# Performance work log

Hardware: AMD Instinct MI355X
Metric: run time of the kernel (lower is better)

## Reference

```python
import jax, jax.numpy as jnp
import numpy as np

B, M, D = 16384, 9, 512
DELTA = 0.5


def setup_inputs() -> dict:
    key = jax.random.key(0)
    k0, k1, k2, k3, k4 = jax.random.split(key, 5)
    s = 1.0 / np.sqrt(D).astype(np.float32)
    return {
        "x": jax.random.normal(k0, (B, M, D), jnp.float32),
        "Wi": jax.random.normal(k1, (M, D, D), jnp.float32) * s,
        "bi": jax.random.normal(k2, (M, D), jnp.float32) * s,
        "We": jax.random.normal(k3, (M, D, D), jnp.float32) * s,
        "be": jax.random.normal(k4, (M, D), jnp.float32) * s,
    }


def reference(x, Wi, bi, We, be):
    # ---- IntraRM: per-branch Linear+Sigmoid, L1-norm gating ----
    # batched per-branch GEMM: [B,M,D] x [M,D,D] -> [B,M,D]
    f = jax.nn.sigmoid(jnp.einsum('bmd,mde->bme', x, Wi) + bi)
    alphas = jnp.sum(jnp.abs(f), axis=-1)          # [B, M]  (L1 norm)
    feats = alphas[:, :, None] * x                  # [B, M, D]
    # ---- InterRM: per-branch Linear+ReLU, cdist affinity, tanh-masked matmul ----
    g = jax.nn.relu(jnp.einsum('bmd,mde->bme', feats, We) + be)  # [B, M, D]
    sq = jnp.sum(g * g, axis=-1)                    # [B, M]
    d2 = sq[:, :, None] + sq[:, None, :] - 2.0 * jnp.einsum('bmd,bnd->bmn', g, g)
    d2 = jnp.maximum(d2, 0.0)
    # safe sqrt (torch.cdist, p=2); diagonal d2==0 handled without NaN grads
    dist = jnp.where(d2 > 0, jnp.sqrt(jnp.where(d2 > 0, d2, 1.0)), 0.0)
    mask = 1.0 - jnp.eye(M, dtype=g.dtype)          # zero self-affinity
    affin = jnp.tanh(dist) * mask                   # [B, M, M]
    g_hat = jnp.einsum('bmn,bnd->bmd', affin, g)    # aggregate across branches
    out = DELTA * g + (1.0 - DELTA) * g_hat
    return out, alphas
```

## Files before the change

kernel.cpp:

```cpp
#include <hip/hip_runtime.h>
#include <hip/hip_bf16.h>
#include <hip/hip_fp16.h>

#define BATCH 16384
#define NM 9
#define ND 512
#define BM 64
#define NKT 16
#define NTHREADS 512
#define WMAT ((size_t)ND * ND)

typedef __bf16 bf16x8 __attribute__((ext_vector_type(8)));
typedef float  f32x4  __attribute__((ext_vector_type(4)));

__global__ __launch_bounds__(256)
void prep_weights(const float* __restrict__ Wi, const float* __restrict__ We,
                  __hip_bfloat16* __restrict__ WiT, __hip_bfloat16* __restrict__ WeT) {
  const int z  = blockIdx.y;
  const int kt = blockIdx.x;
  const float* src;
  __hip_bfloat16* dst;
  if (z < NM) { src = Wi + (size_t)z * WMAT;        dst = WiT + (size_t)z * WMAT; }
  else        { src = We + (size_t)(z - NM) * WMAT; dst = WeT + (size_t)(z - NM) * WMAT; }
  const int wave = threadIdx.x >> 6;
  const int lane = threadIdx.x & 63;
  const int k0   = kt * 32 + (lane >> 4) * 8;
  #pragma unroll
  for (int g = wave; g < 32; g += 4) {
    const int col = g * 16 + (lane & 15);
    bf16x8 v;
    #pragma unroll
    for (int j = 0; j < 8; ++j)
      v[j] = (__bf16)src[(size_t)(k0 + j) * ND + col];
    *(bf16x8*)(dst + (size_t)(kt * 32 + g) * 512 + lane * 8) = v;
  }
}

__global__ __launch_bounds__(NTHREADS, 4)
void gemm_kernel(const float* __restrict__ x,
                 const __hip_bfloat16* __restrict__ WiT,
                 const __hip_bfloat16* __restrict__ WeT,
                 const float* __restrict__ bi,
                 const float* __restrict__ be,
                 float* __restrict__ out) {
  __shared__ union {
    __hip_bfloat16 xs[BM][ND + 8];
    __half         gs[BM][ND + 8];
  } sh;
  __shared__ float alphaW[8][BM];
  __shared__ float alphaV[BM];

  const int tid  = threadIdx.x;
  const int wave = tid >> 6;
  const int lane = tid & 63;
  const int l15  = lane & 15;
  const int l4   = lane >> 4;

  const int bid = blockIdx.x;
  const int q   = bid >> 3;
  const int m   = q >> 5;
  const int bx  = (bid & 7) + ((q & 31) << 3);
  const int b0  = bx * BM;
  const int wn0 = wave * 64;

  float* alpha_out = out + (size_t)BATCH * NM * ND;

  const __hip_bfloat16* bpi = WiT + (size_t)m * WMAT + (size_t)wave * 4 * 512 + lane * 8;
  const __hip_bfloat16* bpe = WeT + (size_t)m * WMAT + (size_t)wave * 4 * 512 + lane * 8;

  bf16x8 breg[3][4];
  bf16x8 afr[2][4];

  #pragma unroll
  for (int d = 0; d < 3; ++d)
    #pragma unroll
    for (int nt = 0; nt < 4; ++nt)
      breg[d][nt] = *(const bf16x8*)(bpi + (size_t)d * 16384 + nt * 512);

  #pragma unroll
  for (int it = 0; it < (BM * ND / 4) / NTHREADS; ++it) {
    int idx = it * NTHREADS + tid;
    int r   = idx >> 7;
    int c4  = (idx & 127) * 4;
    float4 v = *(const float4*)(x + (size_t)(b0 + r) * (NM * ND) + m * ND + c4);
    union { ushort4 u; __hip_bfloat16 h[4]; } p;
    p.h[0] = __float2bfloat16(v.x);
    p.h[1] = __float2bfloat16(v.y);
    p.h[2] = __float2bfloat16(v.z);
    p.h[3] = __float2bfloat16(v.w);
    *(ushort4*)&sh.xs[r][c4] = p.u;
  }
  __syncthreads();

  f32x4 acc[4][4];
  #pragma unroll
  for (int a = 0; a < 4; ++a)
    #pragma unroll
    for (int c = 0; c < 4; ++c) acc[a][c] = (f32x4){0.f, 0.f, 0.f, 0.f};

  #pragma unroll
  for (int mt = 0; mt < 4; ++mt)
    afr[0][mt] = *(const bf16x8*)&sh.xs[mt * 16 + l15][l4 * 8];

  #pragma unroll
  for (int kt = 0; kt < NKT; ++kt) {
    if (kt + 1 < NKT) {
      const int kb = (kt + 1) * 32 + l4 * 8;
      #pragma unroll
      for (int mt = 0; mt < 4; ++mt)
        afr[(kt + 1) & 1][mt] = *(const bf16x8*)&sh.xs[mt * 16 + l15][kb];
    }
    #pragma unroll
    for (int mt = 0; mt < 4; ++mt)
      #pragma unroll
      for (int nt = 0; nt < 4; ++nt)
        acc[mt][nt] = __builtin_amdgcn_mfma_f32_16x16x32_bf16(afr[kt & 1][mt], breg[kt % 3][nt], acc[mt][nt], 0, 0, 0);
    if (kt + 3 < NKT) {
      const size_t off = (size_t)(kt + 3) * 16384;
      #pragma unroll
      for (int nt = 0; nt < 4; ++nt)
        breg[kt % 3][nt] = *(const bf16x8*)(bpi + off + nt * 512);
    }
  }

  #pragma unroll
  for (int d = 0; d < 3; ++d)
    #pragma unroll
    for (int nt = 0; nt < 4; ++nt)
      breg[d][nt] = *(const bf16x8*)(bpe + (size_t)d * 16384 + nt * 512);

  {
    float biv[4];
    #pragma unroll
    for (int nt = 0; nt < 4; ++nt) biv[nt] = bi[m * ND + wn0 + nt * 16 + l15];
    #pragma unroll
    for (int mt = 0; mt < 4; ++mt)
      #pragma unroll
      for (int r = 0; r < 4; ++r) {
        float s = 0.f;
        #pragma unroll
        for (int nt = 0; nt < 4; ++nt) {
          float t = acc[mt][nt][r] + biv[nt];
          s += 1.f / (1.f + __expf(-t));
        }
        s += __shfl_xor(s, 1, 16);
        s += __shfl_xor(s, 2, 16);
        s += __shfl_xor(s, 4, 16);
        s += __shfl_xor(s, 8, 16);
        if (l15 == 0) alphaW[wave][mt * 16 + l4 * 4 + r] = s;
      }
  }

  #pragma unroll
  for (int a = 0; a < 4; ++a)
    #pragma unroll
    for (int c = 0; c < 4; ++c) acc[a][c] = (f32x4){0.f, 0.f, 0.f, 0.f};

  #pragma unroll
  for (int mt = 0; mt < 4; ++mt)
    afr[0][mt] = *(const bf16x8*)&sh.xs[mt * 16 + l15][l4 * 8];

  #pragma unroll
  for (int kt = 0; kt < NKT; ++kt) {
    if (kt + 1 < NKT) {
      const int kb = (kt + 1) * 32 + l4 * 8;
      #pragma unroll
      for (int mt = 0; mt < 4; ++mt)
        afr[(kt + 1) & 1][mt] = *(const bf16x8*)&sh.xs[mt * 16 + l15][kb];
    }
    #pragma unroll
    for (int mt = 0; mt < 4; ++mt)
      #pragma unroll
      for (int nt = 0; nt < 4; ++nt)
        acc[mt][nt] = __builtin_amdgcn_mfma_f32_16x16x32_bf16(afr[kt & 1][mt], breg[kt % 3][nt], acc[mt][nt], 0, 0, 0);
    if (kt + 3 < NKT) {
      const size_t off = (size_t)(kt + 3) * 16384;
      #pragma unroll
      for (int nt = 0; nt < 4; ++nt)
        breg[kt % 3][nt] = *(const bf16x8*)(bpe + off + nt * 512);
    }
  }

  __syncthreads();

  if (tid < BM) {
    float a = 0.f;
    #pragma unroll
    for (int w = 0; w < 8; ++w) a += alphaW[w][tid];
    alphaV[tid] = a;
    alpha_out[(size_t)(b0 + tid) * NM + m] = a;
  }
  __syncthreads();

  {
    float bev[4];
    #pragma unroll
    for (int nt = 0; nt < 4; ++nt) bev[nt] = be[m * ND + wn0 + nt * 16 + l15];
    #pragma unroll
    for (int mt = 0; mt < 4; ++mt)
      #pragma unroll
      for (int r = 0; r < 4; ++r) {
        const int row = mt * 16 + l4 * 4 + r;
        const float al = alphaV[row];
        #pragma unroll
        for (int nt = 0; nt < 4; ++nt) {
          float t = fmaxf(al * acc[mt][nt][r] + bev[nt], 0.f);
          sh.gs[row][wn0 + nt * 16 + l15] = __float2half(t);
        }
      }
    __syncthreads();
    #pragma unroll
    for (int i = 0; i < 8; ++i) {
      const int row = wave + i * 8;
      __half* gd = (__half*)((char*)out + (size_t)(b0 + row) * (NM * ND * 4)) + m * ND;
      *(uint4*)(gd + lane * 8) = *(const uint4*)&sh.gs[row][lane * 8];
    }
  }
}

__global__ __launch_bounds__(256)
void inter_kernel(float* __restrict__ out) {
  __shared__ float gs[NM][ND + 8];
  __shared__ float Gr[45];
  __shared__ float aff[NM][NM];
  const int b = blockIdx.x;
  const int tid = threadIdx.x;
  const __half* gsrc = (const __half*)((const char*)out + (size_t)b * (NM * ND * 4));

  for (int i = tid; i < NM * ND / 4; i += 256) {
    union { ushort4 u; __half h[4]; } p;
    p.u = *(const ushort4*)((const ushort*)gsrc + (size_t)i * 4);
    const int m = i >> 7;
    const int e = (i & 127) * 4;
    #pragma unroll
    for (int j = 0; j < 4; ++j) gs[m][e + j] = __half2float(p.h[j]);
  }
  __syncthreads();

  const int wave = tid >> 6, lane = tid & 63;
  for (int pr = wave; pr < 45; pr += 4) {
    int a = 0, qq = pr;
    while (qq >= NM - a) { qq -= NM - a; ++a; }
    const int bb = a + qq;
    float s = 0.f;
    #pragma unroll
    for (int j = 0; j < 8; ++j) s += gs[a][lane + 64 * j] * gs[bb][lane + 64 * j];
    #pragma unroll
    for (int off = 1; off < 64; off <<= 1) s += __shfl_xor(s, off, 64);
    if (lane == 0) Gr[pr] = s;
  }
  __syncthreads();

  if (tid < NM * NM) {
    const int mm = tid / NM, nn = tid % NM;
    float v = 0.f;
    if (mm != nn) {
      const int a = mm < nn ? mm : nn;
      const int c = mm < nn ? nn : mm;
      auto tri = [](int t) { return t * NM - (t * (t - 1)) / 2; };
      float d2 = Gr[tri(mm)] + Gr[tri(nn)] - 2.f * Gr[tri(a) + (c - a)];
      d2 = fmaxf(d2, 0.f);
      v = tanhf(sqrtf(d2));
    }
    aff[tid / NM][tid % NM] = v;
  }
  __syncthreads();

  float* od = out + (size_t)b * (NM * ND);
  for (int i = tid; i < NM * ND / 4; i += 256) {
    const int mm = i >> 7;
    const int e4 = (i & 127) * 4;
    float4 r;
    #pragma unroll
    for (int j = 0; j < 4; ++j) {
      const int e = e4 + j;
      float acc = 0.f;
      #pragma unroll
      for (int n = 0; n < NM; ++n) acc += aff[mm][n] * gs[n][e];
      ((float*)&r)[j] = 0.5f * (gs[mm][e] + acc);
    }
    *(float4*)(od + (size_t)mm * ND + e4) = r;
  }
}

extern "C" void kernel_launch(void* const* d_in, const int* in_sizes, int n_in,
                              void* d_out, int out_size, void* d_ws, size_t ws_size,
                              hipStream_t stream) {
  const float* x  = (const float*)d_in[0];
  const float* Wi = (const float*)d_in[1];
  const float* bi = (const float*)d_in[2];
  const float* We = (const float*)d_in[3];
  const float* be = (const float*)d_in[4];
  float* out = (float*)d_out;

  __hip_bfloat16* WiT = (__hip_bfloat16*)d_ws;
  __hip_bfloat16* WeT = WiT + (size_t)NM * ND * ND;

  prep_weights<<<dim3(NKT, 2 * NM), 256, 0, stream>>>(Wi, We, WiT, WeT);
  gemm_kernel<<<BATCH / BM * NM, NTHREADS, 0, stream>>>(x, WiT, WeT, bi, be, out);
  inter_kernel<<<BATCH, 256, 0, stream>>>(out);
}
```

Baseline: 371.7 us.

## Stream x tile into LDS per k-step, overlapping global loads with first GEMM

Instead of loading and converting the whole 64x512 x tile into shared memory before the first GEMM, each thread now loads one 32-column chunk per k-step two steps ahead and writes it to LDS during the MFMA loop. This hides global-load latency of x behind the Wi GEMM. The cost is a workgroup barrier every k-step plus explicit lgkmcnt waits, and the A fragments are no longer double-buffered in registers. The second GEMM still reads the full tile afterwards, so that path is unchanged.

After: 756.6 us. 104% more time.

```diff
diff --git a/kernel.cpp b/kernel.cpp
--- a/kernel.cpp
+++ b/kernel.cpp
@@ -12,6 +12,15 @@
 
 typedef __bf16 bf16x8 __attribute__((ext_vector_type(8)));
 typedef float  f32x4  __attribute__((ext_vector_type(4)));
+
+__device__ inline ushort4 cvt4_bf16(float4 v) {
+  union { ushort4 u; __hip_bfloat16 h[4]; } p;
+  p.h[0] = __float2bfloat16(v.x);
+  p.h[1] = __float2bfloat16(v.y);
+  p.h[2] = __float2bfloat16(v.z);
+  p.h[3] = __float2bfloat16(v.w);
+  return p.u;
+}
 
 __global__ __launch_bounds__(256)
 void prep_weights(const float* __restrict__ Wi, const float* __restrict__ We,
@@ -65,32 +74,27 @@
 
   float* alpha_out = out + (size_t)BATCH * NM * ND;
 
+  const int srow = tid >> 3;
+  const int scg  = (tid & 7) * 4;
+  const float* xrow = x + (size_t)(b0 + srow) * (NM * ND) + m * ND + scg;
+
   const __hip_bfloat16* bpi = WiT + (size_t)m * WMAT + (size_t)wave * 4 * 512 + lane * 8;
   const __hip_bfloat16* bpe = WeT + (size_t)m * WMAT + (size_t)wave * 4 * 512 + lane * 8;
 
   bf16x8 breg[3][4];
-  bf16x8 afr[2][4];
-
+
+  float4 L0 = *(const float4*)(xrow);
+  float4 Lh = *(const float4*)(xrow + 32);
   #pragma unroll
   for (int d = 0; d < 3; ++d)
     #pragma unroll
     for (int nt = 0; nt < 4; ++nt)
       breg[d][nt] = *(const bf16x8*)(bpi + (size_t)d * 16384 + nt * 512);
-
-  #pragma unroll
-  for (int it = 0; it < (BM * ND / 4) / NTHREADS; ++it) {
-    int idx = it * NTHREADS + tid;
-    int r   = idx >> 7;
-    int c4  = (idx & 127) * 4;
-    float4 v = *(const float4*)(x + (size_t)(b0 + r) * (NM * ND) + m * ND + c4);
-    union { ushort4 u; __hip_bfloat16 h[4]; } p;
-    p.h[0] = __float2bfloat16(v.x);
-    p.h[1] = __float2bfloat16(v.y);
-    p.h[2] = __float2bfloat16(v.z);
-    p.h[3] = __float2bfloat16(v.w);
-    *(ushort4*)&sh.xs[r][c4] = p.u;
-  }
-  __syncthreads();
+  *(ushort4*)&sh.xs[srow][scg] = cvt4_bf16(L0);
+  asm volatile("s_waitcnt lgkmcnt(0)" ::: "memory");
+  __builtin_amdgcn_sched_barrier(0);
+  __builtin_amdgcn_s_barrier();
+  __builtin_amdgcn_sched_barrier(0);
 
   f32x4 acc[4][4];
   #pragma unroll
@@ -99,28 +103,33 @@
     for (int c = 0; c < 4; ++c) acc[a][c] = (f32x4){0.f, 0.f, 0.f, 0.f};
 
   #pragma unroll
-  for (int mt = 0; mt < 4; ++mt)
-    afr[0][mt] = *(const bf16x8*)&sh.xs[mt * 16 + l15][l4 * 8];
-
-  #pragma unroll
   for (int kt = 0; kt < NKT; ++kt) {
-    if (kt + 1 < NKT) {
-      const int kb = (kt + 1) * 32 + l4 * 8;
-      #pragma unroll
-      for (int mt = 0; mt < 4; ++mt)
-        afr[(kt + 1) & 1][mt] = *(const bf16x8*)&sh.xs[mt * 16 + l15][kb];
-    }
+    float4 Ln;
+    if (kt + 2 < NKT) Ln = *(const float4*)(xrow + (kt + 2) * 32);
+    bf16x8 af[4];
+    const int kbase = kt * 32 + l4 * 8;
+    #pragma unroll
+    for (int mt = 0; mt < 4; ++mt)
+      af[mt] = *(const bf16x8*)&sh.xs[mt * 16 + l15][kbase];
     #pragma unroll
     for (int mt = 0; mt < 4; ++mt)
       #pragma unroll
       for (int nt = 0; nt < 4; ++nt)
-        acc[mt][nt] = __builtin_amdgcn_mfma_f32_16x16x32_bf16(afr[kt & 1][mt], breg[kt % 3][nt], acc[mt][nt], 0, 0, 0);
+        acc[mt][nt] = __builtin_amdgcn_mfma_f32_16x16x32_bf16(af[mt], breg[kt % 3][nt], acc[mt][nt], 0, 0, 0);
     if (kt + 3 < NKT) {
       const size_t off = (size_t)(kt + 3) * 16384;
       #pragma unroll
       for (int nt = 0; nt < 4; ++nt)
         breg[kt % 3][nt] = *(const bf16x8*)(bpi + off + nt * 512);
     }
+    if (kt + 1 < NKT) {
+      *(ushort4*)&sh.xs[srow][(kt + 1) * 32 + scg] = cvt4_bf16(Lh);
+      Lh = Ln;
+    }
+    asm volatile("s_waitcnt lgkmcnt(0)" ::: "memory");
+    __builtin_amdgcn_sched_barrier(0);
+    __builtin_amdgcn_s_barrier();
+    __builtin_amdgcn_sched_barrier(0);
   }
 
   #pragma unroll
@@ -156,6 +165,7 @@
     #pragma unroll
     for (int c = 0; c < 4; ++c) acc[a][c] = (f32x4){0.f, 0.f, 0.f, 0.f};
 
+  bf16x8 afr[2][4];
   #pragma unroll
   for (int mt = 0; mt < 4; ++mt)
     afr[0][mt] = *(const bf16x8*)&sh.xs[mt * 16 + l15][l4 * 8];
```

## Double row tile to 128 and overlap x staging with first GEMM

Applied to the files above, without the earlier changes.

Raises the per-block batch tile from 64 to 128 rows so each weight fragment loaded from global memory feeds twice as many MFMAs, halving weight traffic per output. The second half of the x tile is loaded and converted while the first eight k-steps of the intra GEMM run, hiding part of the staging latency. The weight prefetch depth drops from 3 to 2 and the A-fragment double buffering is removed to fit the larger accumulator set, and occupancy is lowered to 2 blocks per CU with larger shared memory use.

New measurement: 618.3 us. 1.66x slower.

```diff
diff --git a/kernel.cpp b/kernel.cpp
--- a/kernel.cpp
+++ b/kernel.cpp
@@ -5,13 +5,23 @@
 #define BATCH 16384
 #define NM 9
 #define ND 512
-#define BM 64
+#define BM 128
 #define NKT 16
 #define NTHREADS 512
 #define WMAT ((size_t)ND * ND)
+#define XROW (NM * ND)
 
 typedef __bf16 bf16x8 __attribute__((ext_vector_type(8)));
 typedef float  f32x4  __attribute__((ext_vector_type(4)));
+
+__device__ inline ushort4 cvt4_bf16(float4 v) {
+  union { ushort4 u; __hip_bfloat16 h[4]; } p;
+  p.h[0] = __float2bfloat16(v.x);
+  p.h[1] = __float2bfloat16(v.y);
+  p.h[2] = __float2bfloat16(v.z);
+  p.h[3] = __float2bfloat16(v.w);
+  return p.u;
+}
 
 __global__ __launch_bounds__(256)
 void prep_weights(const float* __restrict__ Wi, const float* __restrict__ We,
@@ -36,7 +46,7 @@
   }
 }
 
-__global__ __launch_bounds__(NTHREADS, 4)
+__global__ __launch_bounds__(NTHREADS, 2)
 void gemm_kernel(const float* __restrict__ x,
                  const __hip_bfloat16* __restrict__ WiT,
                  const __hip_bfloat16* __restrict__ WeT,
@@ -58,73 +68,90 @@
 
   const int bid = blockIdx.x;
   const int q   = bid >> 3;
-  const int m   = q >> 5;
-  const int bx  = (bid & 7) + ((q & 31) << 3);
+  const int m   = q >> 4;
+  const int bx  = (bid & 7) + ((q & 15) << 3);
   const int b0  = bx * BM;
   const int wn0 = wave * 64;
 
   float* alpha_out = out + (size_t)BATCH * NM * ND;
 
+  const int srow = tid >> 3;
+  const int scg  = (tid & 7) * 4;
+  const float* xrow0 = x + (size_t)(b0 + srow) * XROW + m * ND + scg;
+
   const __hip_bfloat16* bpi = WiT + (size_t)m * WMAT + (size_t)wave * 4 * 512 + lane * 8;
   const __hip_bfloat16* bpe = WeT + (size_t)m * WMAT + (size_t)wave * 4 * 512 + lane * 8;
 
-  bf16x8 breg[3][4];
-  bf16x8 afr[2][4];
-
-  #pragma unroll
-  for (int d = 0; d < 3; ++d)
+  bf16x8 breg[2][4];
+  #pragma unroll
+  for (int d = 0; d < 2; ++d)
     #pragma unroll
     for (int nt = 0; nt < 4; ++nt)
       breg[d][nt] = *(const bf16x8*)(bpi + (size_t)d * 16384 + nt * 512);
 
   #pragma unroll
-  for (int it = 0; it < (BM * ND / 4) / NTHREADS; ++it) {
-    int idx = it * NTHREADS + tid;
-    int r   = idx >> 7;
-    int c4  = (idx & 127) * 4;
-    float4 v = *(const float4*)(x + (size_t)(b0 + r) * (NM * ND) + m * ND + c4);
-    union { ushort4 u; __hip_bfloat16 h[4]; } p;
-    p.h[0] = __float2bfloat16(v.x);
-    p.h[1] = __float2bfloat16(v.y);
-    p.h[2] = __float2bfloat16(v.z);
-    p.h[3] = __float2bfloat16(v.w);
-    *(ushort4*)&sh.xs[r][c4] = p.u;
-  }
-  __syncthreads();
-
-  f32x4 acc[4][4];
-  #pragma unroll
-  for (int a = 0; a < 4; ++a)
+  for (int rr = 0; rr < 2; ++rr)
+    #pragma unroll
+    for (int j = 0; j < 8; ++j) {
+      float4 v = *(const float4*)(xrow0 + (size_t)rr * 64 * XROW + j * 32);
+      *(ushort4*)&sh.xs[srow + rr * 64][j * 32 + scg] = cvt4_bf16(v);
+    }
+  __syncthreads();
+
+  f32x4 acc[8][4];
+  #pragma unroll
+  for (int a = 0; a < 8; ++a)
     #pragma unroll
     for (int c = 0; c < 4; ++c) acc[a][c] = (f32x4){0.f, 0.f, 0.f, 0.f};
 
   #pragma unroll
-  for (int mt = 0; mt < 4; ++mt)
-    afr[0][mt] = *(const bf16x8*)&sh.xs[mt * 16 + l15][l4 * 8];
-
-  #pragma unroll
-  for (int kt = 0; kt < NKT; ++kt) {
-    if (kt + 1 < NKT) {
-      const int kb = (kt + 1) * 32 + l4 * 8;
-      #pragma unroll
-      for (int mt = 0; mt < 4; ++mt)
-        afr[(kt + 1) & 1][mt] = *(const bf16x8*)&sh.xs[mt * 16 + l15][kb];
-    }
-    #pragma unroll
-    for (int mt = 0; mt < 4; ++mt)
-      #pragma unroll
-      for (int nt = 0; nt < 4; ++nt)
-        acc[mt][nt] = __builtin_amdgcn_mfma_f32_16x16x32_bf16(afr[kt & 1][mt], breg[kt % 3][nt], acc[mt][nt], 0, 0, 0);
-    if (kt + 3 < NKT) {
-      const size_t off = (size_t)(kt + 3) * 16384;
-      #pragma unroll
-      for (int nt = 0; nt < 4; ++nt)
-        breg[kt % 3][nt] = *(const bf16x8*)(bpi + off + nt * 512);
-    }
-  }
-
-  #pragma unroll
-  for (int d = 0; d < 3; ++d)
+  for (int kt = 0; kt < 8; ++kt) {
+    #pragma unroll
+    for (int s2 = 0; s2 < 2; ++s2) {
+      const int idx = kt * 2 + s2;
+      const int rr  = idx >> 3, j = idx & 7;
+      float4 v = *(const float4*)(xrow0 + (size_t)rr * 64 * XROW + 256 + j * 32);
+      *(ushort4*)&sh.xs[srow + rr * 64][256 + j * 32 + scg] = cvt4_bf16(v);
+    }
+    bf16x8 af[8];
+    #pragma unroll
+    for (int mt = 0; mt < 8; ++mt)
+      af[mt] = *(const bf16x8*)&sh.xs[mt * 16 + l15][kt * 32 + l4 * 8];
+    #pragma unroll
+    for (int mt = 0; mt < 8; ++mt)
+      #pragma unroll
+      for (int nt = 0; nt < 4; ++nt)
+        acc[mt][nt] = __builtin_amdgcn_mfma_f32_16x16x32_bf16(af[mt], breg[kt & 1][nt], acc[mt][nt], 0, 0, 0);
+    if (kt + 2 < NKT) {
+      const size_t off = (size_t)(kt + 2) * 16384;
+      #pragma unroll
+      for (int nt = 0; nt < 4; ++nt)
+        breg[kt & 1][nt] = *(const bf16x8*)(bpi + off + nt * 512);
+    }
+  }
+  __syncthreads();
+
+  #pragma unroll
+  for (int kt = 8; kt < NKT; ++kt) {
+    bf16x8 af[8];
+    #pragma unroll
+    for (int mt = 0; mt < 8; ++mt)
+      af[mt] = *(const bf16x8*)&sh.xs[mt * 16 + l15][kt * 32 + l4 * 8];
+    #pragma unroll
+    for (int mt = 0; mt < 8; ++mt)
+      #pragma unroll
+      for (int nt = 0; nt < 4; ++nt)
+        acc[mt][nt] = __builtin_amdgcn_mfma_f32_16x16x32_bf16(af[mt], breg[kt & 1][nt], acc[mt][nt], 0, 0, 0);
+    if (kt + 2 < NKT) {
+      const size_t off = (size_t)(kt + 2) * 16384;
+      #pragma unroll
+      for (int nt = 0; nt < 4; ++nt)
+        breg[kt & 1][nt] = *(const bf16x8*)(bpi + off + nt * 512);
+    }
+  }
+
+  #pragma unroll
+  for (int d = 0; d < 2; ++d)
     #pragma unroll
     for (int nt = 0; nt < 4; ++nt)
       breg[d][nt] = *(const bf16x8*)(bpe + (size_t)d * 16384 + nt * 512);
@@ -134,7 +161,7 @@
     #pragma unroll
     for (int nt = 0; nt < 4; ++nt) biv[nt] = bi[m * ND + wn0 + nt * 16 + l15];
     #pragma unroll
-    for (int mt = 0; mt < 4; ++mt)
+    for (int mt = 0; mt < 8; ++mt)
       #pragma unroll
       for (int r = 0; r < 4; ++r) {
         float s = 0.f;
@@ -152,32 +179,26 @@
   }
 
   #pragma unroll
-  for (int a = 0; a < 4; ++a)
+  for (int a = 0; a < 8; ++a)
     #pragma unroll
     for (int c = 0; c < 4; ++c) acc[a][c] = (f32x4){0.f, 0.f, 0.f, 0.f};
 
   #pragma unroll
-  for (int mt = 0; mt < 4; ++mt)
-    afr[0][mt] = *(const bf16x8*)&sh.xs[mt * 16 + l15][l4 * 8];
-
-  #pragma unroll
   for (int kt = 0; kt < NKT; ++kt) {
-    if (kt + 1 < NKT) {
-      const int kb = (kt + 1) * 32 + l4 * 8;
-      #pragma unroll
-      for (int mt = 0; mt < 4; ++mt)
-        afr[(kt + 1) & 1][mt] = *(const bf16x8*)&sh.xs[mt * 16 + l15][kb];
-    }
-    #pragma unroll
-    for (int mt = 0; mt < 4; ++mt)
-      #pragma unroll
-      for (int nt = 0; nt < 4; ++nt)
-        acc[mt][nt] = __builtin_amdgcn_mfma_f32_16x16x32_bf16(afr[kt & 1][mt], breg[kt % 3][nt], acc[mt][nt], 0, 0, 0);
-    if (kt + 3 < NKT) {
-      const size_t off = (size_t)(kt + 3) * 16384;
-      #pragma unroll
-      for (int nt = 0; nt < 4; ++nt)
-        breg[kt % 3][nt] = *(const bf16x8*)(bpe + off + nt * 512);
+    bf16x8 af[8];
+    #pragma unroll
+    for (int mt = 0; mt < 8; ++mt)
+      af[mt] = *(const bf16x8*)&sh.xs[mt * 16 + l15][kt * 32 + l4 * 8];
+    #pragma unroll
+    for (int mt = 0; mt < 8; ++mt)
+      #pragma unroll
+      for (int nt = 0; nt < 4; ++nt)
+        acc[mt][nt] = __builtin_amdgcn_mfma_f32_16x16x32_bf16(af[mt], breg[kt & 1][nt], acc[mt][nt], 0, 0, 0);
+    if (kt + 2 < NKT) {
+      const size_t off = (size_t)(kt + 2) * 16384;
+      #pragma unroll
+      for (int nt = 0; nt < 4; ++nt)
+        breg[kt & 1][nt] = *(const bf16x8*)(bpe + off + nt * 512);
     }
   }
 
@@ -197,7 +218,7 @@
     #pragma unroll
     for (int nt = 0; nt < 4; ++nt) bev[nt] = be[m * ND + wn0 + nt * 16 + l15];
     #pragma unroll
-    for (int mt = 0; mt < 4; ++mt)
+    for (int mt = 0; mt < 8; ++mt)
       #pragma unroll
       for (int r = 0; r < 4; ++r) {
         const int row = mt * 16 + l4 * 4 + r;
@@ -210,9 +231,9 @@
       }
     __syncthreads();
     #pragma unroll
-    for (int i = 0; i < 8; ++i) {
+    for (int i = 0; i < 16; ++i) {
       const int row = wave + i * 8;
-      __half* gd = (__half*)((char*)out + (size_t)(b0 + row) * (NM * ND * 4)) + m * ND;
+      __half* gd = (__half*)((char*)out + (size_t)(b0 + row) * (XROW * 4)) + m * ND;
       *(uint4*)(gd + lane * 8) = *(const uint4*)&sh.gs[row][lane * 8];
     }
   }
```

## Stage weight slices through LDS with async global_load_lds double buffering

Applied to the files above, without the earlier changes.

Weight K-slices are no longer loaded straight from global memory into registers. They are now copied into a double-buffered LDS area with global_load_lds, and the prefetch runs continuously from the Wi GEMM into the We GEMM. Part of the x tile load is also overlapped with the first K iterations. This should hide weight-load latency and cut register pressure. The cost is about 64KB of extra LDS, a __syncthreads per K step, and lowering launch_bounds occupancy from 4 to 2.

Result: slower. 513.0 us (+38.0%).

```diff
diff --git a/kernel.cpp b/kernel.cpp
--- a/kernel.cpp
+++ b/kernel.cpp
@@ -9,9 +9,19 @@
 #define NKT 16
 #define NTHREADS 512
 #define WMAT ((size_t)ND * ND)
+#define XROW (NM * ND)
 
 typedef __bf16 bf16x8 __attribute__((ext_vector_type(8)));
 typedef float  f32x4  __attribute__((ext_vector_type(4)));
+
+__device__ inline ushort4 cvt4_bf16(float4 v) {
+  union { ushort4 u; __hip_bfloat16 h[4]; } p;
+  p.h[0] = __float2bfloat16(v.x);
+  p.h[1] = __float2bfloat16(v.y);
+  p.h[2] = __float2bfloat16(v.z);
+  p.h[3] = __float2bfloat16(v.w);
+  return p.u;
+}
 
 __global__ __launch_bounds__(256)
 void prep_weights(const float* __restrict__ Wi, const float* __restrict__ We,
@@ -36,7 +46,7 @@
   }
 }
 
-__global__ __launch_bounds__(NTHREADS, 4)
+__global__ __launch_bounds__(NTHREADS, 2)
 void gemm_kernel(const float* __restrict__ x,
                  const __hip_bfloat16* __restrict__ WiT,
                  const __hip_bfloat16* __restrict__ WeT,
@@ -47,6 +57,7 @@
     __hip_bfloat16 xs[BM][ND + 8];
     __half         gs[BM][ND + 8];
   } sh;
+  __shared__ __align__(16) __hip_bfloat16 Bs[2][16384];
   __shared__ float alphaW[8][BM];
   __shared__ float alphaV[BM];
 
@@ -65,69 +76,72 @@
 
   float* alpha_out = out + (size_t)BATCH * NM * ND;
 
-  const __hip_bfloat16* bpi = WiT + (size_t)m * WMAT + (size_t)wave * 4 * 512 + lane * 8;
-  const __hip_bfloat16* bpe = WeT + (size_t)m * WMAT + (size_t)wave * 4 * 512 + lane * 8;
-
-  bf16x8 breg[3][4];
-  bf16x8 afr[2][4];
-
-  #pragma unroll
-  for (int d = 0; d < 3; ++d)
-    #pragma unroll
-    for (int nt = 0; nt < 4; ++nt)
-      breg[d][nt] = *(const bf16x8*)(bpi + (size_t)d * 16384 + nt * 512);
-
-  #pragma unroll
-  for (int it = 0; it < (BM * ND / 4) / NTHREADS; ++it) {
-    int idx = it * NTHREADS + tid;
-    int r   = idx >> 7;
-    int c4  = (idx & 127) * 4;
-    float4 v = *(const float4*)(x + (size_t)(b0 + r) * (NM * ND) + m * ND + c4);
-    union { ushort4 u; __hip_bfloat16 h[4]; } p;
-    p.h[0] = __float2bfloat16(v.x);
-    p.h[1] = __float2bfloat16(v.y);
-    p.h[2] = __float2bfloat16(v.z);
-    p.h[3] = __float2bfloat16(v.w);
-    *(ushort4*)&sh.xs[r][c4] = p.u;
-  }
-  __syncthreads();
-
-  f32x4 acc[4][4];
-  #pragma unroll
-  for (int a = 0; a < 4; ++a)
-    #pragma unroll
-    for (int c = 0; c < 4; ++c) acc[a][c] = (f32x4){0.f, 0.f, 0.f, 0.f};
-
+  const __hip_bfloat16* wiB = WiT + (size_t)m * WMAT;
+  const __hip_bfloat16* weB = WeT + (size_t)m * WMAT;
+
+  auto stage = [&](const __hip_bfloat16* wb, int buf, int slice) {
+    const __hip_bfloat16* src = wb + (size_t)slice * 16384 + tid * 8;
+    #pragma unroll
+    for (int j = 0; j < 4; ++j)
+      __builtin_amdgcn_global_load_lds(
+          (const __attribute__((address_space(1))) unsigned int*)(src + j * 4096),
+          (__attribute__((address_space(3))) unsigned int*)(&Bs[buf][j * 4096 + tid * 8]),
+          16, 0, 0);
+  };
+
+  const int srow = tid >> 3;
+  const int scg  = (tid & 7) * 4;
+  const float* xrow0 = x + (size_t)(b0 + srow) * XROW + m * ND + scg;
+
+  stage(wiB, 0, 0);
+  stage(wiB, 1, 1);
+  #pragma unroll
+  for (int s = 0; s < 8; ++s) {
+    float4 v = *(const float4*)(xrow0 + s * 32);
+    *(ushort4*)&sh.xs[srow][s * 32 + scg] = cvt4_bf16(v);
+  }
+  float4 xh0 = *(const float4*)(xrow0 + 8 * 32);
+  float4 xh1 = *(const float4*)(xrow0 + 9 * 32);
+  __syncthreads();
+
+  bf16x8 afr[2][4], bfr[2][4];
+  #pragma unroll
+  for (int nt = 0; nt < 4; ++nt)
+    bfr[0][nt] = *(const bf16x8*)&Bs[0][(wave * 4 + nt) * 512 + lane * 8];
   #pragma unroll
   for (int mt = 0; mt < 4; ++mt)
     afr[0][mt] = *(const bf16x8*)&sh.xs[mt * 16 + l15][l4 * 8];
 
+  f32x4 acc[4][4];
+  #pragma unroll
+  for (int a = 0; a < 4; ++a)
+    #pragma unroll
+    for (int c = 0; c < 4; ++c) acc[a][c] = (f32x4){0.f, 0.f, 0.f, 0.f};
+
   #pragma unroll
   for (int kt = 0; kt < NKT; ++kt) {
+    __syncthreads();
+    if (kt < 14) stage(wiB, kt & 1, kt + 2);
+    else         stage(weB, kt & 1, kt - 14);
+    if (kt < 8) {
+      *(ushort4*)&sh.xs[srow][(8 + kt) * 32 + scg] = cvt4_bf16(xh0);
+      xh0 = xh1;
+      if (kt < 6) xh1 = *(const float4*)(xrow0 + (10 + kt) * 32);
+    }
     if (kt + 1 < NKT) {
-      const int kb = (kt + 1) * 32 + l4 * 8;
+      #pragma unroll
+      for (int nt = 0; nt < 4; ++nt)
+        bfr[(kt + 1) & 1][nt] = *(const bf16x8*)&Bs[(kt + 1) & 1][(wave * 4 + nt) * 512 + lane * 8];
       #pragma unroll
       for (int mt = 0; mt < 4; ++mt)
-        afr[(kt + 1) & 1][mt] = *(const bf16x8*)&sh.xs[mt * 16 + l15][kb];
+        afr[(kt + 1) & 1][mt] = *(const bf16x8*)&sh.xs[mt * 16 + l15][(kt + 1) * 32 + l4 * 8];
     }
     #pragma unroll
     for (int mt = 0; mt < 4; ++mt)
       #pragma unroll
       for (int nt = 0; nt < 4; ++nt)
-        acc[mt][nt] = __builtin_amdgcn_mfma_f32_16x16x32_bf16(afr[kt & 1][mt], breg[kt % 3][nt], acc[mt][nt], 0, 0, 0);
-    if (kt + 3 < NKT) {
-      const size_t off = (size_t)(kt + 3) * 16384;
-      #pragma unroll
-      for (int nt = 0; nt < 4; ++nt)
-        breg[kt % 3][nt] = *(const bf16x8*)(bpi + off + nt * 512);
-    }
-  }
-
-  #pragma unroll
-  for (int d = 0; d < 3; ++d)
-    #pragma unroll
-    for (int nt = 0; nt < 4; ++nt)
-      breg[d][nt] = *(const bf16x8*)(bpe + (size_t)d * 16384 + nt * 512);
+        acc[mt][nt] = __builtin_amdgcn_mfma_f32_16x16x32_bf16(afr[kt & 1][mt], bfr[kt & 1][nt], acc[mt][nt], 0, 0, 0);
+  }
 
   {
     float biv[4];
@@ -152,33 +166,34 @@
   }
 
   #pragma unroll
-  for (int a = 0; a < 4; ++a)
-    #pragma unroll
-    for (int c = 0; c < 4; ++c) acc[a][c] = (f32x4){0.f, 0.f, 0.f, 0.f};
-
+  for (int nt = 0; nt < 4; ++nt)
+    bfr[0][nt] = *(const bf16x8*)&Bs[0][(wave * 4 + nt) * 512 + lane * 8];
   #pragma unroll
   for (int mt = 0; mt < 4; ++mt)
     afr[0][mt] = *(const bf16x8*)&sh.xs[mt * 16 + l15][l4 * 8];
 
   #pragma unroll
+  for (int a = 0; a < 4; ++a)
+    #pragma unroll
+    for (int c = 0; c < 4; ++c) acc[a][c] = (f32x4){0.f, 0.f, 0.f, 0.f};
+
+  #pragma unroll
   for (int kt = 0; kt < NKT; ++kt) {
+    __syncthreads();
+    if (kt + 2 < NKT) stage(weB, kt & 1, kt + 2);
     if (kt + 1 < NKT) {
-      const int kb = (kt + 1) * 32 + l4 * 8;
+      #pragma unroll
+      for (int nt = 0; nt < 4; ++nt)
+        bfr[(kt + 1) & 1][nt] = *(const bf16x8*)&Bs[(kt + 1) & 1][(wave * 4 + nt) * 512 + lane * 8];
       #pragma unroll
       for (int mt = 0; mt < 4; ++mt)
-        afr[(kt + 1) & 1][mt] = *(const bf16x8*)&sh.xs[mt * 16 + l15][kb];
+        afr[(kt + 1) & 1][mt] = *(const bf16x8*)&sh.xs[mt * 16 + l15][(kt + 1) * 32 + l4 * 8];
     }
     #pragma unroll
     for (int mt = 0; mt < 4; ++mt)
       #pragma unroll
       for (int nt = 0; nt < 4; ++nt)
-        acc[mt][nt] = __builtin_amdgcn_mfma_f32_16x16x32_bf16(afr[kt & 1][mt], breg[kt % 3][nt], acc[mt][nt], 0, 0, 0);
-    if (kt + 3 < NKT) {
-      const size_t off = (size_t)(kt + 3) * 16384;
-      #pragma unroll
-      for (int nt = 0; nt < 4; ++nt)
-        breg[kt % 3][nt] = *(const bf16x8*)(bpe + off + nt * 512);
-    }
+        acc[mt][nt] = __builtin_amdgcn_mfma_f32_16x16x32_bf16(afr[kt & 1][mt], bfr[kt & 1][nt], acc[mt][nt], 0, 0, 0);
   }
 
   __syncthreads();
@@ -212,7 +227,7 @@
     #pragma unroll
     for (int i = 0; i < 8; ++i) {
       const int row = wave + i * 8;
-      __half* gd = (__half*)((char*)out + (size_t)(b0 + row) * (NM * ND * 4)) + m * ND;
+      __half* gd = (__half*)((char*)out + (size_t)(b0 + row) * (XROW * 4)) + m * ND;
       *(uint4*)(gd + lane * 8) = *(const uint4*)&sh.gs[row][lane * 8];
     }
   }
```
